# Performance work log

Hardware: AMD Instinct MI355X
Metric: run time of the kernel (lower is better)

Reference implementation:

```python
import jax, jax.numpy as jnp
import numpy as np

B_SZ = 8
D_MODEL = 512
D_STATE = 64
N2 = D_STATE // 2  # S4D uses complex-conjugate pairs -> d_state//2 complex modes
L_SEQ = 2048


def setup_inputs() -> dict:
    key = jax.random.key(0)
    ks = jax.random.split(key, 16)
    d = D_MODEL
    scale = 1.0 / np.sqrt(d)
    inp = {
        "x": jax.random.normal(ks[0], (B_SZ, d, L_SEQ), dtype=jnp.float32),
        # q/k/v projections (nn.Linear: weight (out,in), bias (out,))
        "Wq": jax.random.normal(ks[1], (d, d), dtype=jnp.float32) * scale,
        "bq": jax.random.normal(ks[2], (d,), dtype=jnp.float32) * scale,
        "Wk": jax.random.normal(ks[3], (d, d), dtype=jnp.float32) * scale,
        "bk": jax.random.normal(ks[4], (d,), dtype=jnp.float32) * scale,
        "Wv": jax.random.normal(ks[5], (d, d), dtype=jnp.float32) * scale,
        "bv": jax.random.normal(ks[6], (d,), dtype=jnp.float32) * scale,
        # Shift layer params
        "shift_C": jax.random.normal(ks[7], (1, d, D_STATE), dtype=jnp.float32),
        "shift_D": jax.random.normal(ks[8], (d,), dtype=jnp.float32),
        # S4D (diagonal SSM) params
        "log_dt": jax.random.uniform(ks[9], (d,), dtype=jnp.float32,
                                      minval=np.log(1e-3), maxval=np.log(1e-1)),
        "A_real": jnp.log(0.5 * jnp.ones((d, N2), dtype=jnp.float32)),
        "A_imag": jnp.broadcast_to(np.pi * jnp.arange(N2, dtype=jnp.float32), (d, N2)),
        "C_re": jax.random.normal(ks[10], (d, N2), dtype=jnp.float32) * np.sqrt(0.5),
        "C_im": jax.random.normal(ks[11], (d, N2), dtype=jnp.float32) * np.sqrt(0.5),
        "s4_D": jax.random.normal(ks[12], (d,), dtype=jnp.float32),
    }
    return inp


def _linear_chan(x, W, b):
    # x: (B, H, L); Linear applied over channel dim H -> (B, H_out, L)
    return jnp.einsum("bhl,dh->bdl", x, W) + b[:, None]


def _shift(u, C, Dp):
    """Shift SSM: causal conv with kernel = first L taps of C (computed via FFT
    exactly as the torch source does). u: (B, H, L)."""
    L = u.shape[-1]
    n = 2 * L
    H, S = C.shape[1], C.shape[2]
    Bmat = jnp.zeros((H, S), dtype=u.dtype).at[:, 0].set(1.0)
    B_fc = jnp.conj(jnp.fft.rfft(Bmat, n=n, axis=-1))  # (H, L+1)
    C_f = jnp.fft.rfft(C, n=n, axis=-1)                # (1, H, L+1)
    kernel = jnp.fft.irfft(B_fc * C_f, n=n, axis=-1)[..., :L]  # (1, H, L)
    kernel_f = jnp.fft.rfft(kernel, n=n, axis=-1)      # (1, H, L+1)
    u_f = jnp.fft.rfft(u, n=n, axis=-1)                # (B, H, L+1)
    y = jnp.fft.irfft(u_f * kernel_f, n=n, axis=-1)[..., :L]
    return y + u * Dp[:, None]


def _s4d(u, log_dt, A_real, A_imag, C_re, C_im, Dp):
    """Standard S4D forward: ZOH-discretized diagonal SSM kernel + FFT conv.
    u: (B, H, L)."""
    L = u.shape[-1]
    n = 2 * L
    dt = jnp.exp(log_dt)[:, None]                  # (H, 1)
    A = -jnp.exp(A_real) + 1j * A_imag             # (H, N2)
    dtA = A * dt                                   # (H, N2)
    C = (C_re + 1j * C_im) * (jnp.exp(dtA) - 1.0) / A
    vand = jnp.exp(dtA[:, :, None] * jnp.arange(L))  # (H, N2, L)
    K = 2.0 * jnp.einsum("hn,hnl->hl", C, vand).real  # (H, L)
    y = jnp.fft.irfft(jnp.fft.rfft(u, n=n, axis=-1) * jnp.fft.rfft(K, n=n, axis=-1),
                      n=n, axis=-1)[..., :L]
    return y + u * Dp[:, None]


def reference(x, Wq, bq, Wk, bk, Wv, bv, shift_C, shift_D,
              log_dt, A_real, A_imag, C_re, C_im, s4_D):
    q = _linear_chan(x, Wq, bq)
    k = _linear_chan(x, Wk, bk)
    v = _linear_chan(x, Wv, bv)
    shift_out = _shift(k, shift_C, shift_D)
    s4d_out = _s4d(v * shift_out, log_dt, A_real, A_imag, C_re, C_im, s4_D)
    return q * s4d_out
```

## Files before the change

kernel.cpp:

```cpp
#include <hip/hip_runtime.h>
#include <cstdint>


#define DMODEL 512
#define LSEQ 2048

typedef _Float16 half_t;
typedef __attribute__((ext_vector_type(2))) _Float16 half2v;
typedef __attribute__((ext_vector_type(4))) _Float16 half4v;
typedef __attribute__((ext_vector_type(8))) _Float16 half8v;
typedef __attribute__((ext_vector_type(4))) float floatx4;

#define SW(R, c) ((R) * 64 + ((((c) >> 3) ^ ((R) & 7)) << 3) + ((c) & 7))

__device__ __forceinline__ void gload_lds16(const half_t* g, half_t* l) {
  __builtin_amdgcn_global_load_lds(
      (const __attribute__((address_space(1))) uint32_t*)g,
      (__attribute__((address_space(3))) uint32_t*)l, 16, 0, 0);
}

#define WAIT_LGKM_BAR()                                   \
  do {                                                    \
    asm volatile("s_waitcnt lgkmcnt(0)" ::: "memory");    \
    __builtin_amdgcn_s_barrier();                         \
    __builtin_amdgcn_sched_barrier(0);                    \
  } while (0)

__global__ __launch_bounds__(256) void prep(
    const float* __restrict__ x, const float* __restrict__ Wq,
    const float* __restrict__ Wk, const float* __restrict__ Wv,
    const float* __restrict__ log_dt, const float* __restrict__ A_real,
    const float* __restrict__ A_imag, const float* __restrict__ C_re,
    const float* __restrict__ C_im, const float* __restrict__ shC,
    half_t* __restrict__ xT, half_t* __restrict__ W16,
    half_t* __restrict__ Vt, half_t* __restrict__ Et, half_t* __restrict__ Tt,
    half_t* __restrict__ T1t, half_t* __restrict__ T2t,
    float* __restrict__ wt2) {
  __shared__ float tile[64][68];
  __shared__ float aL[32], bL[32], wrL[32], wiL[32], crL[32], ciL[32];
  __shared__ float Kt[64], tapl[64];
  int bid = blockIdx.x;
  int tid = threadIdx.x;

  if (bid < 512) {
    int h = bid;
    if (tid < 64) { Kt[tid] = 0.f; tapl[tid] = shC[h * 64 + tid]; }
    if (tid < 32) {
      int n = tid, hn = h * 32 + n;
      float dt = expf(log_dt[h]);
      float Ar = -expf(A_real[hn]), Ai = A_imag[hn];
      float a = dt * Ar, b = dt * Ai;
      float ea = expf(a);
      float wr = ea * cosf(b), wi = ea * sinf(b);
      float Am2 = Ar * Ar + Ai * Ai;
      float zr = wr - 1.0f, zi = wi;
      float qr = (zr * Ar + zi * Ai) / Am2;
      float qi = (zi * Ar - zr * Ai) / Am2;
      aL[n] = a; bL[n] = b; wrL[n] = wr; wiL[n] = wi;
      crL[n] = C_re[hn] * qr - C_im[hn] * qi;
      ciL[n] = C_re[hn] * qi + C_im[hn] * qr;
      float e64 = expf(64.0f * a);
      wt2[h * 64 + 2 * n]     = e64 * cosf(64.0f * b);
      wt2[h * 64 + 2 * n + 1] = e64 * sinf(64.0f * b);
    }
    __syncthreads();
    size_t base = (size_t)h * 4096;
    {
      int r = tid >> 2;
      int nb = (tid & 3) * 8;
      float ksum = 0.f;
#pragma unroll
      for (int i = 0; i < 8; i++) {
        int n = nb + i;
        float a = aL[n], b = bL[n];
        float cr = crL[n], ci = ciL[n];
        float er = expf(a * (float)r);
        float w0r = er * cosf(b * (float)r), w0i = er * sinf(b * (float)r);
        ksum += 2.f * (cr * w0r - ci * w0i);
        float wr = wrL[n], wi = wiL[n];
        float w1r = w0r * wr - w0i * wi, w1i = w0r * wi + w0i * wr;
        Et[base + SW(r, 2 * n)]     = (half_t)(2.f * (cr * w1r - ci * w1i));
        Et[base + SW(r, 2 * n + 1)] = (half_t)(-2.f * (cr * w1i + ci * w1r));
        Vt[base + SW(2 * n, 63 - r)]     = (half_t)w0r;
        Vt[base + SW(2 * n + 1, 63 - r)] = (half_t)w0i;
      }
      atomicAdd(&Kt[r], ksum);
    }
    __syncthreads();
#pragma unroll
    for (int e = 0; e < 16; e++) {
      int idx = e * 256 + tid;
      int r = idx >> 6, t = idx & 63;
      int d = r - t;
      size_t a = base + SW(r, t);
      Tt[a]  = (d >= 0) ? (half_t)Kt[d] : (half_t)0.f;
      T1t[a] = (d >= 0) ? (half_t)tapl[d] : (half_t)0.f;
      T2t[a] = (d < 0) ? (half_t)tapl[64 + d] : (half_t)0.f;
    }
  } else if (bid < 2560) {
    int i = bid - 512;
    int b = i >> 8, rem = i & 255;
    int d0 = (rem >> 5) * 64, l0 = (rem & 31) * 64;
    int dy = tid >> 4, lx = tid & 15;
    const float* xp = x + ((size_t)(b * 512 + d0)) * 2048 + l0;
#pragma unroll
    for (int rr = 0; rr < 4; rr++) {
      float4 v = *(const float4*)(xp + (size_t)(rr * 16 + dy) * 2048 + lx * 4);
      *(float4*)&tile[rr * 16 + dy][lx * 4] = v;
    }
    __syncthreads();
    half_t* op = xT + ((size_t)(b * 2048 + l0)) * 512 + d0;
    int lr = tid >> 2, c4 = tid & 3;
#pragma unroll
    for (int cc = 0; cc < 2; cc++) {
      int ch = cc * 4 + c4;
      half8v hv;
#pragma unroll
      for (int e = 0; e < 8; e++) hv[e] = (half_t)tile[ch * 8 + e][lr];
      *(half8v*)(op + (size_t)lr * 512 + ch * 8) = hv;
    }
  } else {
    int base = (bid - 2560) * 256 + tid;
#pragma unroll
    for (int it = 0; it < 6; it++) {
      int i = base + it * 131072;
      const float* src = (i < 262144) ? Wq : ((i < 524288) ? Wk : Wv);
      W16[i] = (half_t)src[i & 262143];
    }
  }
}

__global__ __launch_bounds__(256) void gemm_qkv(
    const half_t* __restrict__ xT, const half_t* __restrict__ Wstk,
    const float* __restrict__ bq, const float* __restrict__ bk,
    const float* __restrict__ bv, half_t* __restrict__ outq,
    half_t* __restrict__ outk, half_t* __restrict__ outv) {
  __shared__ half_t smem[16384];
  half_t* As = smem;
  half_t* Bs = smem + 8192;
  int flat = blockIdx.x;
  int swz = (flat & 7) * 192 + (flat >> 3);
  int nt = swz / 12, mt = swz - nt * 12;
  int n0 = nt * 128, m0 = mt * 128;
  int tid = threadIdx.x;
  int lane = tid & 63, wid = tid >> 6;
  int wr = wid >> 1, wc = wid & 1;
  int lrow = lane & 15, lg = lane >> 4;
  int rsub = lane >> 3, ssub = lane & 7;
  int gslot = ssub ^ rsub;

  floatx4 acc[4][4];
#pragma unroll
  for (int i = 0; i < 4; i++)
#pragma unroll
    for (int j = 0; j < 4; j++) acc[i][j] = (floatx4){0.f, 0.f, 0.f, 0.f};

  const half_t* gA = Wstk + (size_t)(m0 + wid * 32 + rsub) * 512 + gslot * 8;
  const half_t* gB = xT + (size_t)(n0 + wid * 32 + rsub) * 512 + gslot * 8;

  for (int kk = 0; kk < 512; kk += 64) {
#pragma unroll
    for (int i = 0; i < 4; i++) {
      int c = wid * 4 + i;
      gload_lds16(gA + (size_t)i * 8 * 512 + kk, As + c * 512);
      gload_lds16(gB + (size_t)i * 8 * 512 + kk, Bs + c * 512);
    }
    __syncthreads();
#pragma unroll
    for (int h = 0; h < 2; h++) {
      half8v af[4], bf[4];
#pragma unroll
      for (int i = 0; i < 4; i++) {
        int r = wr * 64 + i * 16 + lrow;
        af[i] = *(const half8v*)(As + r * 64 + ((h * 4 + lg) ^ (r & 7)) * 8);
      }
#pragma unroll
      for (int j = 0; j < 4; j++) {
        int r = wc * 64 + j * 16 + lrow;
        bf[j] = *(const half8v*)(Bs + r * 64 + ((h * 4 + lg) ^ (r & 7)) * 8);
      }
#pragma unroll
      for (int i = 0; i < 4; i++)
#pragma unroll
        for (int j = 0; j < 4; j++)
          acc[i][j] = __builtin_amdgcn_mfma_f32_16x16x32_f16(af[i], bf[j],
                                                             acc[i][j], 0, 0, 0);
    }
    __syncthreads();
  }

  int z = m0 >> 9;
  const float* bias = (z == 0) ? bq : ((z == 1) ? bk : bv);
  half_t* smemC = smem;
#pragma unroll
  for (int i = 0; i < 4; i++) {
    int dl = wr * 64 + i * 16 + 4 * lg;
    float4 b4 = *(const float4*)&bias[(m0 + dl) & 511];
#pragma unroll
    for (int j = 0; j < 4; j++) {
      int ll = wc * 64 + j * 16 + lrow;
#pragma unroll
      for (int reg = 0; reg < 4; reg++) {
        int d = dl + reg;
        float val = acc[i][j][reg] + ((const float*)&b4)[reg];
        smemC[d * 128 + (((ll >> 3) ^ (d & 15)) << 3) + (ll & 7)] = (half_t)val;
      }
    }
  }
  __syncthreads();
  {
    int t4 = tid >> 4, ch = tid & 15;
    int b = n0 >> 11, l0 = n0 & 2047;
    half_t* outp = (z == 0) ? outq : ((z == 1) ? outk : outv);
#pragma unroll
    for (int rep = 0; rep < 8; rep++) {
      int d = rep * 16 + t4;
      half8v v = *(const half8v*)(smemC + d * 128 + ((ch ^ (d & 15)) << 3));
      size_t rowb = ((size_t)(b * 512 + ((m0 + d) & 511))) * 2048;
      if (z == 0) {
        *(half8v*)(outp + rowb + l0 + ch * 8) = v;
      } else {
        int j = (l0 >> 6) + (ch >> 3);
        int s = ch & 7;
        *(half8v*)(outp + rowb + j * 64 + ((s ^ (j & 7)) << 3)) = v;
      }
    }
  }
}

__global__ __launch_bounds__(512) void s4d_main(
    const half_t* __restrict__ kimg, const half_t* __restrict__ vimg,
    const half_t* __restrict__ T1t, const half_t* __restrict__ T2t,
    const half_t* __restrict__ Vt, const half_t* __restrict__ Et,
    const half_t* __restrict__ Tt, const float* __restrict__ wt2,
    const float* __restrict__ shD, const float* __restrict__ s4D,
    const half_t* __restrict__ qbuf, float* __restrict__ outp) {
  extern __shared__ char smem_raw[];
  half_t* tabA = (half_t*)smem_raw;
  half_t* tabB = tabA + 4096;
  half_t* tabC = tabB + 4096;
  half_t* klb  = tabC + 4096;
  half_t* vgb  = klb + 2 * 2112;
  half_t* uhb  = vgb + 2 * 2048;
  float*  SGb  = (float*)(uhb + 2 * 2048);
  int swz = (blockIdx.x & 7) * 256 + (blockIdx.x >> 3);
  int h = swz >> 2, bp = swz & 3;
  int tid = threadIdx.x;
  int lane = tid & 63, wid = tid >> 6;
  int g = wid >> 2, w4 = wid & 3;
  int tid4 = tid & 255;
  int bi = bp * 2 + g;
  int bh = bi * 512 + h;
  int lrow = lane & 15, lg = lane >> 4;
  int mi = w4 & 1, ri0 = w4 >> 1;
  half_t* klg = klb + g * 2112;
  half_t* vgg = vgb + g * 2048;
  half_t* uhg = uhb + g * 2048;
  float*  SGg = SGb + g * 2112;

  {
    size_t tb = (size_t)h * 4096;
    gload_lds16(kimg + (size_t)bh * 2048 + w4 * 512 + lane * 8,
                klg + 64 + w4 * 512);
    gload_lds16(vimg + (size_t)bh * 2048 + w4 * 512 + lane * 8,
                vgg + w4 * 512);
    gload_lds16(T1t + tb + wid * 512 + lane * 8, tabA + wid * 512);
    gload_lds16(T2t + tb + wid * 512 + lane * 8, tabB + wid * 512);
    gload_lds16(Vt  + tb + wid * 512 + lane * 8, tabC + wid * 512);
  }
  if (tid4 < 8) {
    half8v zz = {(_Float16)0, (_Float16)0, (_Float16)0, (_Float16)0,
                 (_Float16)0, (_Float16)0, (_Float16)0, (_Float16)0};
    *(half8v*)(klg + tid4 * 8) = zz;
  }
  float sDsh = shD[h];
  float sD4 = s4D[h];
  float wTr = wt2[h * 64 + 2 * (tid4 & 31)];
  float wTi = wt2[h * 64 + 2 * (tid4 & 31) + 1];
  asm volatile("s_waitcnt vmcnt(0) lgkmcnt(0)" ::: "memory");
  __builtin_amdgcn_s_barrier();
  __builtin_amdgcn_sched_barrier(0);

#define LDF(base, r, ks, key) \
  (*(const half8v*)((base) + (r) * 64 + (((ks) * 4 + lg) ^ (key)) * 8))

  floatx4 acc[2];
  acc[0] = (floatx4){0.f, 0.f, 0.f, 0.f};
  acc[1] = (floatx4){0.f, 0.f, 0.f, 0.f};
  {
    int jA = mi * 16 + lrow;
    int key1 = lrow & 7, key2 = (lrow + 7) & 7;
#pragma unroll
    for (int ks = 0; ks < 2; ks++) {
      half8v a1 = LDF(klg, 1 + jA, ks, key1);
      half8v a2 = LDF(klg, jA, ks, key2);
#pragma unroll
      for (int tt = 0; tt < 2; tt++) {
        int rb = (ri0 + tt * 2) * 16 + lrow;
        half8v b1 = LDF(tabA, rb, ks, lrow & 7);
        half8v b2 = LDF(tabB, rb, ks, lrow & 7);
        acc[tt] = __builtin_amdgcn_mfma_f32_16x16x32_f16(a1, b1, acc[tt], 0, 0, 0);
        acc[tt] = __builtin_amdgcn_mfma_f32_16x16x32_f16(a2, b2, acc[tt], 0, 0, 0);
      }
    }
  }
#pragma unroll
  for (int tt = 0; tt < 2; tt++) {
#pragma unroll
    for (int reg = 0; reg < 4; reg++) {
      int j = mi * 16 + 4 * lg + reg;
      int r = (ri0 + tt * 2) * 16 + lrow;
      int cph = (((r >> 3) ^ (j & 7)) << 3) + (r & 7);
      float kvv = (float)klg[(1 + j) * 64 + cph];
      float vvv = (float)vgg[j * 64 + cph];
      uhg[j * 64 + cph] = (half_t)(vvv * (acc[tt][reg] + sDsh * kvv));
    }
  }
  WAIT_LGKM_BAR();

  {
    size_t tb = (size_t)h * 4096;
    gload_lds16(Et + tb + wid * 512 + lane * 8, tabA + wid * 512);
    gload_lds16(Tt + tb + wid * 512 + lane * 8, tabB + wid * 512);
  }

  acc[0] = (floatx4){0.f, 0.f, 0.f, 0.f};
  acc[1] = (floatx4){0.f, 0.f, 0.f, 0.f};
#pragma unroll
  for (int ks = 0; ks < 2; ks++) {
    half8v a = LDF(uhg, mi * 16 + lrow, ks, lrow & 7);
#pragma unroll
    for (int tt = 0; tt < 2; tt++) {
      int rb = (ri0 + tt * 2) * 16 + lrow;
      half8v b = LDF(tabC, rb, ks, lrow & 7);
      acc[tt] = __builtin_amdgcn_mfma_f32_16x16x32_f16(a, b, acc[tt], 0, 0, 0);
    }
  }
#pragma unroll
  for (int tt = 0; tt < 2; tt++) {
    int ri = ri0 + tt * 2;
#pragma unroll
    for (int reg = 0; reg < 4; reg++) {
      int j = mi * 16 + 4 * lg + reg;
      SGg[j * 66 + ri * 16 + lrow] = acc[tt][reg];
    }
  }
  asm volatile("s_waitcnt vmcnt(0) lgkmcnt(0)" ::: "memory");
  __builtin_amdgcn_s_barrier();
  __builtin_amdgcn_sched_barrier(0);

  if (tid4 < 32) {
    int n = tid4;
    float gr = 0.f, gi = 0.f;
#pragma unroll 4
    for (int j = 0; j < 32; j++) {
      float tr = SGg[j * 66 + 2 * n], ti = SGg[j * 66 + 2 * n + 1];
      half2v gp = {(half_t)gr, (half_t)gi};
      *(half2v*)(vgg + j * 64 + (((n >> 2) ^ (j & 7)) << 3) + 2 * (n & 3)) = gp;
      float nr = wTr * gr - wTi * gi + tr;
      gi = wTr * gi + wTi * gr + ti;
      gr = nr;
    }
  }
  WAIT_LGKM_BAR();

  acc[0] = (floatx4){0.f, 0.f, 0.f, 0.f};
  acc[1] = (floatx4){0.f, 0.f, 0.f, 0.f};
#pragma unroll
  for (int ks = 0; ks < 2; ks++) {
    half8v ag = LDF(vgg, mi * 16 + lrow, ks, lrow & 7);
    half8v au = LDF(uhg, mi * 16 + lrow, ks, lrow & 7);
#pragma unroll
    for (int tt = 0; tt < 2; tt++) {
      int rb = (ri0 + tt * 2) * 16 + lrow;
      half8v be = LDF(tabA, rb, ks, lrow & 7);
      half8v bt = LDF(tabB, rb, ks, lrow & 7);
      acc[tt] = __builtin_amdgcn_mfma_f32_16x16x32_f16(ag, be, acc[tt], 0, 0, 0);
      acc[tt] = __builtin_amdgcn_mfma_f32_16x16x32_f16(au, bt, acc[tt], 0, 0, 0);
    }
  }
#pragma unroll
  for (int tt = 0; tt < 2; tt++) {
#pragma unroll
    for (int reg = 0; reg < 4; reg++) {
      int j = mi * 16 + 4 * lg + reg;
      int r = (ri0 + tt * 2) * 16 + lrow;
      int cph = (((r >> 3) ^ (j & 7)) << 3) + (r & 7);
      SGg[j * 64 + r] = acc[tt][reg] + sD4 * (float)uhg[j * 64 + cph];
    }
  }
  WAIT_LGKM_BAR();

  {
    size_t base = (size_t)bh * 2048;
    half8v qv = *(const half8v*)(qbuf + base + tid4 * 8);
    float* op = outp + base;
    float4 o0, o1;
    o0.x = (float)qv[0] * SGg[tid4 * 8 + 0];
    o0.y = (float)qv[1] * SGg[tid4 * 8 + 1];
    o0.z = (float)qv[2] * SGg[tid4 * 8 + 2];
    o0.w = (float)qv[3] * SGg[tid4 * 8 + 3];
    o1.x = (float)qv[4] * SGg[tid4 * 8 + 4];
    o1.y = (float)qv[5] * SGg[tid4 * 8 + 5];
    o1.z = (float)qv[6] * SGg[tid4 * 8 + 6];
    o1.w = (float)qv[7] * SGg[tid4 * 8 + 7];
    *(float4*)(op + tid4 * 8) = o0;
    *(float4*)(op + tid4 * 8 + 4) = o1;
  }
#undef LDF
}

extern "C" void kernel_launch(void* const* d_in, const int* in_sizes, int n_in,
                              void* d_out, int out_size, void* d_ws, size_t ws_size,
                              hipStream_t stream) {
  const float* x      = (const float*)d_in[0];
  const float* Wq     = (const float*)d_in[1];
  const float* bq     = (const float*)d_in[2];
  const float* Wk     = (const float*)d_in[3];
  const float* bk     = (const float*)d_in[4];
  const float* Wv     = (const float*)d_in[5];
  const float* bv     = (const float*)d_in[6];
  const float* shC    = (const float*)d_in[7];
  const float* shD    = (const float*)d_in[8];
  const float* log_dt = (const float*)d_in[9];
  const float* A_real = (const float*)d_in[10];
  const float* A_imag = (const float*)d_in[11];
  const float* C_re   = (const float*)d_in[12];
  const float* C_im   = (const float*)d_in[13];
  const float* s4D    = (const float*)d_in[14];
  float* out = (float*)d_out;
  half_t* wsh = (half_t*)d_ws;

  half_t* qbuf = wsh;
  half_t* kbuf = wsh + 8388608;
  half_t* vbuf = wsh + 16777216;
  half_t* xT16 = wsh + 25165824;
  half_t* W16  = wsh + 33554432;
  half_t* Vt   = wsh + 34340864;
  half_t* Et   = wsh + 36438016;
  half_t* Tt   = wsh + 38535168;
  half_t* T1t  = wsh + 40632320;
  half_t* T2t  = wsh + 42729472;
  float*  wt2  = (float*)(wsh + 44826624);

  hipFuncSetAttribute((const void*)s4d_main,
                      hipFuncAttributeMaxDynamicSharedMemorySize, 66304);

  prep<<<3072, 256, 0, stream>>>(x, Wq, Wk, Wv, log_dt, A_real, A_imag,
                                 C_re, C_im, shC, xT16, W16,
                                 Vt, Et, Tt, T1t, T2t, wt2);
  gemm_qkv<<<dim3(1536), 256, 0, stream>>>(xT16, W16, bq, bk, bv,
                                           qbuf, kbuf, vbuf);
  s4d_main<<<dim3(2048), 512, 66304, stream>>>(kbuf, vbuf, T1t, T2t, Vt, Et,
                                               Tt, wt2, shD, s4D, qbuf, out);
}
```

Baseline: 85.39 us.

## Fuse x transpose and fp16 conversion into QKV GEMM B-tile loads

Removes the prep-kernel stage that transposed x into an fp16 (B,L,H) buffer. The GEMM now loads fp32 x directly with vector loads, converts it to fp16 in registers and scatters it into the swizzled LDS B tile. This drops one full write and read of the transposed activation buffer and shrinks the prep grid. The cost is that each of the 12 M-tiles sharing an N-tile re-reads fp32 x (twice the bytes of fp16). It also replaces async global-to-LDS loads with synchronous register loads and many small 4-byte LDS stores, which may slow the GEMM main loop.

Result: slower. 105.7 us (+23.8%).

```diff
diff --git a/kernel.cpp b/kernel.cpp
--- a/kernel.cpp
+++ b/kernel.cpp
@@ -27,16 +27,15 @@
   } while (0)
 
 __global__ __launch_bounds__(256) void prep(
-    const float* __restrict__ x, const float* __restrict__ Wq,
-    const float* __restrict__ Wk, const float* __restrict__ Wv,
+    const float* __restrict__ Wq, const float* __restrict__ Wk,
+    const float* __restrict__ Wv,
     const float* __restrict__ log_dt, const float* __restrict__ A_real,
     const float* __restrict__ A_imag, const float* __restrict__ C_re,
     const float* __restrict__ C_im, const float* __restrict__ shC,
-    half_t* __restrict__ xT, half_t* __restrict__ W16,
+    half_t* __restrict__ W16,
     half_t* __restrict__ Vt, half_t* __restrict__ Et, half_t* __restrict__ Tt,
     half_t* __restrict__ T1t, half_t* __restrict__ T2t,
     float* __restrict__ wt2) {
-  __shared__ float tile[64][68];
   __shared__ float aL[32], bL[32], wrL[32], wiL[32], crL[32], ciL[32];
   __shared__ float Kt[64], tapl[64];
   int bid = blockIdx.x;
@@ -97,30 +96,8 @@
       T1t[a] = (d >= 0) ? (half_t)tapl[d] : (half_t)0.f;
       T2t[a] = (d < 0) ? (half_t)tapl[64 + d] : (half_t)0.f;
     }
-  } else if (bid < 2560) {
-    int i = bid - 512;
-    int b = i >> 8, rem = i & 255;
-    int d0 = (rem >> 5) * 64, l0 = (rem & 31) * 64;
-    int dy = tid >> 4, lx = tid & 15;
-    const float* xp = x + ((size_t)(b * 512 + d0)) * 2048 + l0;
-#pragma unroll
-    for (int rr = 0; rr < 4; rr++) {
-      float4 v = *(const float4*)(xp + (size_t)(rr * 16 + dy) * 2048 + lx * 4);
-      *(float4*)&tile[rr * 16 + dy][lx * 4] = v;
-    }
-    __syncthreads();
-    half_t* op = xT + ((size_t)(b * 2048 + l0)) * 512 + d0;
-    int lr = tid >> 2, c4 = tid & 3;
-#pragma unroll
-    for (int cc = 0; cc < 2; cc++) {
-      int ch = cc * 4 + c4;
-      half8v hv;
-#pragma unroll
-      for (int e = 0; e < 8; e++) hv[e] = (half_t)tile[ch * 8 + e][lr];
-      *(half8v*)(op + (size_t)lr * 512 + ch * 8) = hv;
-    }
   } else {
-    int base = (bid - 2560) * 256 + tid;
+    int base = (bid - 512) * 256 + tid;
 #pragma unroll
     for (int it = 0; it < 6; it++) {
       int i = base + it * 131072;
@@ -131,7 +108,7 @@
 }
 
 __global__ __launch_bounds__(256) void gemm_qkv(
-    const half_t* __restrict__ xT, const half_t* __restrict__ Wstk,
+    const float* __restrict__ x, const half_t* __restrict__ Wstk,
     const float* __restrict__ bq, const float* __restrict__ bk,
     const float* __restrict__ bv, half_t* __restrict__ outq,
     half_t* __restrict__ outk, half_t* __restrict__ outv) {
@@ -148,6 +125,8 @@
   int lrow = lane & 15, lg = lane >> 4;
   int rsub = lane >> 3, ssub = lane & 7;
   int gslot = ssub ^ rsub;
+  int bB = n0 >> 11, l0g = n0 & 2047;
+  int hp = tid >> 3, lsg = tid & 7;
 
   floatx4 acc[4][4];
 #pragma unroll
@@ -156,14 +135,30 @@
     for (int j = 0; j < 4; j++) acc[i][j] = (floatx4){0.f, 0.f, 0.f, 0.f};
 
   const half_t* gA = Wstk + (size_t)(m0 + wid * 32 + rsub) * 512 + gslot * 8;
-  const half_t* gB = xT + (size_t)(n0 + wid * 32 + rsub) * 512 + gslot * 8;
+  const float* gX = x + ((size_t)(bB * 512 + hp * 2)) * 2048 + l0g + lsg * 16;
 
   for (int kk = 0; kk < 512; kk += 64) {
 #pragma unroll
     for (int i = 0; i < 4; i++) {
       int c = wid * 4 + i;
       gload_lds16(gA + (size_t)i * 8 * 512 + kk, As + c * 512);
-      gload_lds16(gB + (size_t)i * 8 * 512 + kk, Bs + c * 512);
+    }
+    {
+      const float* xs = gX + (size_t)kk * 2048;
+      floatx4 r0[4], r1[4];
+#pragma unroll
+      for (int i = 0; i < 4; i++) {
+        r0[i] = *(const floatx4*)(xs + i * 4);
+        r1[i] = *(const floatx4*)(xs + 2048 + i * 4);
+      }
+      int h0 = hp * 2;
+      int colbase = (h0 & 7);
+#pragma unroll
+      for (int i = 0; i < 16; i++) {
+        int ll = lsg * 16 + i;
+        half2v pr = {(half_t)r0[i >> 2][i & 3], (half_t)r1[i >> 2][i & 3]};
+        *(half2v*)(Bs + ll * 64 + ((((h0 >> 3) ^ (ll & 7)) << 3) + colbase)) = pr;
+      }
     }
     __syncthreads();
 #pragma unroll
@@ -210,17 +205,16 @@
   __syncthreads();
   {
     int t4 = tid >> 4, ch = tid & 15;
-    int b = n0 >> 11, l0 = n0 & 2047;
     half_t* outp = (z == 0) ? outq : ((z == 1) ? outk : outv);
 #pragma unroll
     for (int rep = 0; rep < 8; rep++) {
       int d = rep * 16 + t4;
       half8v v = *(const half8v*)(smemC + d * 128 + ((ch ^ (d & 15)) << 3));
-      size_t rowb = ((size_t)(b * 512 + ((m0 + d) & 511))) * 2048;
+      size_t rowb = ((size_t)(bB * 512 + ((m0 + d) & 511))) * 2048;
       if (z == 0) {
-        *(half8v*)(outp + rowb + l0 + ch * 8) = v;
+        *(half8v*)(outp + rowb + l0g + ch * 8) = v;
       } else {
-        int j = (l0 >> 6) + (ch >> 3);
+        int j = (l0g >> 6) + (ch >> 3);
         int s = ch & 7;
         *(half8v*)(outp + rowb + j * 64 + ((s ^ (j & 7)) << 3)) = v;
       }
@@ -434,22 +428,21 @@
   half_t* qbuf = wsh;
   half_t* kbuf = wsh + 8388608;
   half_t* vbuf = wsh + 16777216;
-  half_t* xT16 = wsh + 25165824;
-  half_t* W16  = wsh + 33554432;
-  half_t* Vt   = wsh + 34340864;
-  half_t* Et   = wsh + 36438016;
-  half_t* Tt   = wsh + 38535168;
-  half_t* T1t  = wsh + 40632320;
-  half_t* T2t  = wsh + 42729472;
-  float*  wt2  = (float*)(wsh + 44826624);
+  half_t* W16  = wsh + 25165824;
+  half_t* Vt   = wsh + 25952256;
+  half_t* Et   = wsh + 28049408;
+  half_t* Tt   = wsh + 30146560;
+  half_t* T1t  = wsh + 32243712;
+  half_t* T2t  = wsh + 34340864;
+  float*  wt2  = (float*)(wsh + 36438016);
 
   hipFuncSetAttribute((const void*)s4d_main,
                       hipFuncAttributeMaxDynamicSharedMemorySize, 66304);
 
-  prep<<<3072, 256, 0, stream>>>(x, Wq, Wk, Wv, log_dt, A_real, A_imag,
-                                 C_re, C_im, shC, xT16, W16,
+  prep<<<1024, 256, 0, stream>>>(Wq, Wk, Wv, log_dt, A_real, A_imag,
+                                 C_re, C_im, shC, W16,
                                  Vt, Et, Tt, T1t, T2t, wt2);
-  gemm_qkv<<<dim3(1536), 256, 0, stream>>>(xT16, W16, bq, bk, bv,
+  gemm_qkv<<<dim3(1536), 256, 0, stream>>>(x, W16, bq, bk, bv,
                                            qbuf, kbuf, vbuf);
   s4d_main<<<dim3(2048), 512, 66304, stream>>>(kbuf, vbuf, T1t, T2t, Vt, Et,
                                                Tt, wt2, shD, s4D, qbuf, out);
```
